# Optimization experiments

Measured on AMD Instinct MI355X. Metric: run time of the kernel, lower is better.

## Reference

```python
import jax, jax.numpy as jnp
import numpy as np

DEGREE = 12      # number of interior basis control dims
ORDER = 3        # cubic B-spline
V = 10           # number_variables
N = 65536        # batch
L = V * (V - 1) // 2          # 45 lambdas (strict lower triangle)
NCOEF = DEGREE + ORDER - 1    # 14 coefficients per lambda
LO, HI = -5.0, 5.0            # spline_range[:,0]


def make_knots():
    d = (HI - LO) / (DEGREE - 1)
    return jnp.linspace(LO - ORDER * d, HI + ORDER * d, DEGREE + 2 * ORDER, dtype=jnp.float32)


def bspline_basis(x, knots):
    # Cox-de Boor recursion, vectorized over all leading dims of x.
    # returns [..., NCOEF] basis values (len(knots) - ORDER - 1 functions).
    t = knots
    xe = x[..., None]
    B = ((xe >= t[:-1]) & (xe < t[1:])).astype(x.dtype)  # order-0 indicators
    for p in range(1, ORDER + 1):
        d1 = t[p:-1] - t[:-p - 1]
        d2 = t[p + 1:] - t[1:-p]
        a = jnp.where(d1 > 0, (xe - t[:-p - 1]) / jnp.where(d1 > 0, d1, 1.0), 0.0)
        b = jnp.where(d2 > 0, (t[p + 1:] - xe) / jnp.where(d2 > 0, d2, 1.0), 0.0)
        B = a * B[..., :-1] + b * B[..., 1:]
    return B


def setup_inputs() -> dict:
    key = jax.random.key(0)
    k1, k2 = jax.random.split(key)
    x = jax.random.normal(k1, (N, V), dtype=jnp.float32) * 2.0
    log_d = jnp.zeros((N, V), dtype=jnp.float32)
    params = 0.001 + 0.01 * jax.random.normal(k2, (NCOEF, L), dtype=jnp.float32)
    return {"x": x, "log_d": log_d, "params": params}


def reference(x, log_d, params):
    knots = make_knots()
    rows, cols = np.tril_indices(V, k=-1)  # var_num_list, covar_num_list
    # ReLULeR span restriction: clamp inputs into the spline range
    xc = jnp.clip(x[:, cols], LO, HI)              # [N, L]
    B = bspline_basis(xc, knots)                    # [N, L, NCOEF]
    lam = jnp.einsum('nlk,kl->nl', B, params)       # de Boor evaluation per pair
    # triangular lambda matrix: identity + scattered strict-lower entries
    eye = jnp.eye(V, dtype=x.dtype)
    M = jnp.broadcast_to(eye, (x.shape[0], V, V)).at[:, rows, cols].set(lam)
    out = jnp.einsum('nij,nj->ni', M, x)            # bmm(lambda_matrix, input)
    # ridge penalties on spline coefficients (penalize_towards=0)
    sec = jnp.sum(jnp.diff(params, n=2, axis=0) ** 2)
    fir = jnp.sum(jnp.diff(params, n=1, axis=0) ** 2)
    par = jnp.sum(params ** 2)
    return out, M, log_d, sec, fir, par
```

## Files before the change

### kernel.cpp

```cpp
#include <hip/hip_runtime.h>

#define V 10
#define L 45
#define NCOEF 14
#define NSAMP 65536
#define BS 32
#define LAMP 48

typedef float v4f __attribute__((ext_vector_type(4)));

__constant__ unsigned char c_col[L] = {
    0,
    0,1,
    0,1,2,
    0,1,2,3,
    0,1,2,3,4,
    0,1,2,3,4,5,
    0,1,2,3,4,5,6,
    0,1,2,3,4,5,6,7,
    0,1,2,3,4,5,6,7,8
};

__global__ __launch_bounds__(256) void decor_fused(
    const float* __restrict__ x, const float* __restrict__ log_d,
    const float* __restrict__ params,
    float* __restrict__ out, float* __restrict__ Mout, float* __restrict__ logd_out,
    float* __restrict__ scal)
{
    __shared__ float ps[NCOEF * L];
    __shared__ int   cols[L];
    __shared__ float xs[BS * V];
    __shared__ float lam[BS * LAMP];
    __shared__ float os[BS * V];

    const int tid = threadIdx.x;
    const int n0  = blockIdx.x * BS;

    for (int idx = tid; idx < NCOEF * L; idx += 256)
        ps[idx] = params[idx];
    if (tid < L) cols[tid] = c_col[tid];

    const v4f* x4 = (const v4f*)(x + (size_t)n0 * V);
    for (int idx = tid; idx < BS * V / 4; idx += 256)
        ((v4f*)xs)[idx] = __builtin_nontemporal_load(&x4[idx]);

    const v4f* ld4  = (const v4f*)(log_d + (size_t)n0 * V);
    v4f*       ldo4 = (v4f*)(logd_out + (size_t)n0 * V);
    for (int idx = tid; idx < BS * V / 4; idx += 256)
        __builtin_nontemporal_store(__builtin_nontemporal_load(&ld4[idx]), &ldo4[idx]);

    __syncthreads();

    const float inv_d = 1.1f;
    const float c16   = 1.0f / 6.0f;
    for (int idx = tid; idx < BS * L; idx += 256) {
        int nl = idx / L;
        int l  = idx - nl * L;
        float xv = xs[nl * V + cols[l]];
        xv = fminf(fmaxf(xv, -5.0f), 5.0f);
        float u  = (xv + 5.0f) * inv_d + 3.0f;
        int   ii = (int)floorf(u);
        ii = max(3, min(ii, 14));
        float f  = u - (float)ii;
        float omf = 1.0f - f;
        float f2 = f * f, f3 = f2 * f;
        float N0 = omf * omf * omf * c16;
        float N1 = (3.0f * f3 - 6.0f * f2 + 4.0f) * c16;
        float N2 = (-3.0f * f3 + 3.0f * f2 + 3.0f * f + 1.0f) * c16;
        float N3 = f3 * c16;
        int k0 = ii - 3;
        int k3 = min(k0 + 3, NCOEF - 1);
        lam[nl * LAMP + l] =
              N0 * ps[(k0    ) * L + l]
            + N1 * ps[(k0 + 1) * L + l]
            + N2 * ps[(k0 + 2) * L + l]
            + N3 * ps[(k3    ) * L + l];
    }
    __syncthreads();

    v4f* M4 = (v4f*)(Mout + (size_t)n0 * V * V);
    for (int idx = tid; idx < BS * 25; idx += 256) {
        int nl = idx / 25;
        int q  = idx - nl * 25;
        int e  = q * 4;
        const float* lr = &lam[nl * LAMP];
        v4f v;
        #pragma unroll
        for (int t = 0; t < 4; ++t) {
            int ee = e + t;
            int i  = (ee * 205) >> 11;
            int j  = ee - 10 * i;
            float val;
            if (j > i)       val = 0.0f;
            else if (j == i) val = 1.0f;
            else             val = lr[(i * (i - 1)) / 2 + j];
            v[t] = val;
        }
        __builtin_nontemporal_store(v, &M4[idx]);
    }

    for (int idx = tid; idx < BS * V; idx += 256) {
        int nl = idx / V;
        int i  = idx - nl * V;
        float acc = xs[idx];
        const float* lr = &lam[nl * LAMP + (i * (i - 1)) / 2];
        for (int j = 0; j < i; ++j)
            acc += lr[j] * xs[nl * V + j];
        os[idx] = acc;
    }
    __syncthreads();

    v4f* o4 = (v4f*)(out + (size_t)n0 * V);
    for (int idx = tid; idx < BS * V / 4; idx += 256)
        __builtin_nontemporal_store(((const v4f*)os)[idx], &o4[idx]);

    if (blockIdx.x == 0 && tid < 64) {
        float s_par = 0.f, s_fir = 0.f, s_sec = 0.f;
        for (int idx = tid; idx < NCOEF * L; idx += 64) {
            int k = idx / L;
            float p0 = ps[idx];
            s_par += p0 * p0;
            if (k + 1 < NCOEF) {
                float p1 = ps[idx + L];
                float d1 = p1 - p0;
                s_fir += d1 * d1;
                if (k + 2 < NCOEF) {
                    float p2 = ps[idx + 2 * L];
                    float d2 = p2 - 2.f * p1 + p0;
                    s_sec += d2 * d2;
                }
            }
        }
        for (int off = 32; off; off >>= 1) {
            s_sec += __shfl_down(s_sec, off);
            s_fir += __shfl_down(s_fir, off);
            s_par += __shfl_down(s_par, off);
        }
        if (tid == 0) { scal[0] = s_sec; scal[1] = s_fir; scal[2] = s_par; }
    }
}

extern "C" void kernel_launch(void* const* d_in, const int* in_sizes, int n_in,
                              void* d_out, int out_size, void* d_ws, size_t ws_size,
                              hipStream_t stream) {
    const float* x      = (const float*)d_in[0];
    const float* log_d  = (const float*)d_in[1];
    const float* params = (const float*)d_in[2];

    float* out      = (float*)d_out;
    float* M        = out + (size_t)NSAMP * V;
    float* logd_out = M + (size_t)NSAMP * V * V;
    float* scal     = logd_out + (size_t)NSAMP * V;

    decor_fused<<<NSAMP / BS, 256, 0, stream>>>(x, log_d, params, out, M, logd_out, scal);
}
```

Before: 17.75 us.

## Write M directly from lambda loop with scalar stores and halve block size

The vectorised M-matrix write pass is replaced by two kinds of scalar stores. The diagonal and upper-triangle constants are written up front, and each lambda is stored to M directly where it is computed. The output staging buffer and one barrier are removed, nontemporal loads and stores become plain accesses, and the block shrinks to 128 threads with an occupancy hint. This aims to cut a shared-memory pass and a sync. In exchange, the M stores become uncoalesced scalar writes instead of 16-byte vector stores, which may hurt write bandwidth on the dominant output.

```diff
diff --git a/kernel.cpp b/kernel.cpp
--- a/kernel.cpp
+++ b/kernel.cpp
@@ -5,58 +5,67 @@
 #define NCOEF 14
 #define NSAMP 65536
 #define BS 32
-#define LAMP 48
+#define NTHR 128
+#define LAMP 46
 
 typedef float v4f __attribute__((ext_vector_type(4)));
 
-__constant__ unsigned char c_col[L] = {
-    0,
-    0,1,
-    0,1,2,
-    0,1,2,3,
-    0,1,2,3,4,
-    0,1,2,3,4,5,
-    0,1,2,3,4,5,6,
-    0,1,2,3,4,5,6,7,
-    0,1,2,3,4,5,6,7,8
+__constant__ unsigned char c_ij[L] = {
+    0x10,
+    0x20,0x21,
+    0x30,0x31,0x32,
+    0x40,0x41,0x42,0x43,
+    0x50,0x51,0x52,0x53,0x54,
+    0x60,0x61,0x62,0x63,0x64,0x65,
+    0x70,0x71,0x72,0x73,0x74,0x75,0x76,
+    0x80,0x81,0x82,0x83,0x84,0x85,0x86,0x87,
+    0x90,0x91,0x92,0x93,0x94,0x95,0x96,0x97,0x98
 };
 
-__global__ __launch_bounds__(256) void decor_fused(
+__global__ __launch_bounds__(NTHR, 8) void decor_fused(
     const float* __restrict__ x, const float* __restrict__ log_d,
     const float* __restrict__ params,
     float* __restrict__ out, float* __restrict__ Mout, float* __restrict__ logd_out,
     float* __restrict__ scal)
 {
     __shared__ float ps[NCOEF * L];
-    __shared__ int   cols[L];
     __shared__ float xs[BS * V];
     __shared__ float lam[BS * LAMP];
-    __shared__ float os[BS * V];
+    __shared__ unsigned char ij[48];
 
     const int tid = threadIdx.x;
     const int n0  = blockIdx.x * BS;
+    float* __restrict__ Mb = Mout + (size_t)n0 * V * V;
 
-    for (int idx = tid; idx < NCOEF * L; idx += 256)
+    for (int idx = tid; idx < NCOEF * L; idx += NTHR)
         ps[idx] = params[idx];
-    if (tid < L) cols[tid] = c_col[tid];
+    const v4f* x4 = (const v4f*)(x + (size_t)n0 * V);
+    for (int idx = tid; idx < BS * V / 4; idx += NTHR)
+        ((v4f*)xs)[idx] = x4[idx];
+    if (tid < L) ij[tid] = c_ij[tid];
 
-    const v4f* x4 = (const v4f*)(x + (size_t)n0 * V);
-    for (int idx = tid; idx < BS * V / 4; idx += 256)
-        ((v4f*)xs)[idx] = __builtin_nontemporal_load(&x4[idx]);
+    for (int idx = tid; idx < BS * V * V; idx += NTHR) {
+        int e = idx % (V * V);
+        int i = (e * 205) >> 11;
+        int j = e - 10 * i;
+        if (j >= i) Mb[idx] = (j == i) ? 1.0f : 0.0f;
+    }
 
     const v4f* ld4  = (const v4f*)(log_d + (size_t)n0 * V);
     v4f*       ldo4 = (v4f*)(logd_out + (size_t)n0 * V);
-    for (int idx = tid; idx < BS * V / 4; idx += 256)
-        __builtin_nontemporal_store(__builtin_nontemporal_load(&ld4[idx]), &ldo4[idx]);
+    for (int idx = tid; idx < BS * V / 4; idx += NTHR)
+        ldo4[idx] = ld4[idx];
 
     __syncthreads();
 
     const float inv_d = 1.1f;
     const float c16   = 1.0f / 6.0f;
-    for (int idx = tid; idx < BS * L; idx += 256) {
+    for (int idx = tid; idx < BS * L; idx += NTHR) {
         int nl = idx / L;
         int l  = idx - nl * L;
-        float xv = xs[nl * V + cols[l]];
+        int pij = ij[l];
+        int i = pij >> 4, j = pij & 15;
+        float xv = xs[nl * V + j];
         xv = fminf(fmaxf(xv, -5.0f), 5.0f);
         float u  = (xv + 5.0f) * inv_d + 3.0f;
         int   ii = (int)floorf(u);
@@ -70,49 +79,26 @@
         float N3 = f3 * c16;
         int k0 = ii - 3;
         int k3 = min(k0 + 3, NCOEF - 1);
-        lam[nl * LAMP + l] =
+        float lv =
               N0 * ps[(k0    ) * L + l]
             + N1 * ps[(k0 + 1) * L + l]
             + N2 * ps[(k0 + 2) * L + l]
             + N3 * ps[(k3    ) * L + l];
+        lam[nl * LAMP + l] = lv;
+        Mb[nl * V * V + i * V + j] = lv;
     }
+
     __syncthreads();
 
-    v4f* M4 = (v4f*)(Mout + (size_t)n0 * V * V);
-    for (int idx = tid; idx < BS * 25; idx += 256) {
-        int nl = idx / 25;
-        int q  = idx - nl * 25;
-        int e  = q * 4;
-        const float* lr = &lam[nl * LAMP];
-        v4f v;
-        #pragma unroll
-        for (int t = 0; t < 4; ++t) {
-            int ee = e + t;
-            int i  = (ee * 205) >> 11;
-            int j  = ee - 10 * i;
-            float val;
-            if (j > i)       val = 0.0f;
-            else if (j == i) val = 1.0f;
-            else             val = lr[(i * (i - 1)) / 2 + j];
-            v[t] = val;
-        }
-        __builtin_nontemporal_store(v, &M4[idx]);
-    }
-
-    for (int idx = tid; idx < BS * V; idx += 256) {
+    for (int idx = tid; idx < BS * V; idx += NTHR) {
         int nl = idx / V;
         int i  = idx - nl * V;
         float acc = xs[idx];
         const float* lr = &lam[nl * LAMP + (i * (i - 1)) / 2];
         for (int j = 0; j < i; ++j)
             acc += lr[j] * xs[nl * V + j];
-        os[idx] = acc;
+        out[(size_t)n0 * V + idx] = acc;
     }
-    __syncthreads();
-
-    v4f* o4 = (v4f*)(out + (size_t)n0 * V);
-    for (int idx = tid; idx < BS * V / 4; idx += 256)
-        __builtin_nontemporal_store(((const v4f*)os)[idx], &o4[idx]);
 
     if (blockIdx.x == 0 && tid < 64) {
         float s_par = 0.f, s_fir = 0.f, s_sec = 0.f;
@@ -152,5 +138,5 @@
     float* logd_out = M + (size_t)NSAMP * V * V;
     float* scal     = logd_out + (size_t)NSAMP * V;
 
-    decor_fused<<<NSAMP / BS, 256, 0, stream>>>(x, log_d, params, out, M, logd_out, scal);
+    decor_fused<<<NSAMP / BS, NTHR, 0, stream>>>(x, log_d, params, out, M, logd_out, scal);
 }
```

New measurement: 20.12 us. +13.4%, slower.

## Fuse spline evaluation into M-matrix write and shrink blocks to 16 samples

Applied to the files above, without the earlier changes.

Computes each lambda inline while writing the M matrix and drops the separate lambda pass and one barrier. The output is now stored directly instead of being staged through shared memory. Block size drops from 32 to 16 samples with 128 threads, and launch bounds are set to allow more resident blocks. The aim is fewer barriers and lower shared-memory use per block, at the cost of twice as many blocks each reloading the params table and scalar, uncoalesced output stores.

```diff
diff --git a/kernel.cpp b/kernel.cpp
--- a/kernel.cpp
+++ b/kernel.cpp
@@ -4,86 +4,44 @@
 #define L 45
 #define NCOEF 14
 #define NSAMP 65536
-#define BS 32
-#define LAMP 48
+#define BS 16
+#define NTHR 128
+#define LAMP 46
 
 typedef float v4f __attribute__((ext_vector_type(4)));
 
-__constant__ unsigned char c_col[L] = {
-    0,
-    0,1,
-    0,1,2,
-    0,1,2,3,
-    0,1,2,3,4,
-    0,1,2,3,4,5,
-    0,1,2,3,4,5,6,
-    0,1,2,3,4,5,6,7,
-    0,1,2,3,4,5,6,7,8
-};
-
-__global__ __launch_bounds__(256) void decor_fused(
+__global__ __launch_bounds__(NTHR, 8) void decor_fused(
     const float* __restrict__ x, const float* __restrict__ log_d,
     const float* __restrict__ params,
     float* __restrict__ out, float* __restrict__ Mout, float* __restrict__ logd_out,
     float* __restrict__ scal)
 {
     __shared__ float ps[NCOEF * L];
-    __shared__ int   cols[L];
     __shared__ float xs[BS * V];
     __shared__ float lam[BS * LAMP];
-    __shared__ float os[BS * V];
 
     const int tid = threadIdx.x;
     const int n0  = blockIdx.x * BS;
 
-    for (int idx = tid; idx < NCOEF * L; idx += 256)
+    for (int idx = tid; idx < NCOEF * L; idx += NTHR)
         ps[idx] = params[idx];
-    if (tid < L) cols[tid] = c_col[tid];
-
     const v4f* x4 = (const v4f*)(x + (size_t)n0 * V);
-    for (int idx = tid; idx < BS * V / 4; idx += 256)
+    for (int idx = tid; idx < BS * V / 4; idx += NTHR)
         ((v4f*)xs)[idx] = __builtin_nontemporal_load(&x4[idx]);
-
     const v4f* ld4  = (const v4f*)(log_d + (size_t)n0 * V);
     v4f*       ldo4 = (v4f*)(logd_out + (size_t)n0 * V);
-    for (int idx = tid; idx < BS * V / 4; idx += 256)
+    for (int idx = tid; idx < BS * V / 4; idx += NTHR)
         __builtin_nontemporal_store(__builtin_nontemporal_load(&ld4[idx]), &ldo4[idx]);
 
     __syncthreads();
 
     const float inv_d = 1.1f;
     const float c16   = 1.0f / 6.0f;
-    for (int idx = tid; idx < BS * L; idx += 256) {
-        int nl = idx / L;
-        int l  = idx - nl * L;
-        float xv = xs[nl * V + cols[l]];
-        xv = fminf(fmaxf(xv, -5.0f), 5.0f);
-        float u  = (xv + 5.0f) * inv_d + 3.0f;
-        int   ii = (int)floorf(u);
-        ii = max(3, min(ii, 14));
-        float f  = u - (float)ii;
-        float omf = 1.0f - f;
-        float f2 = f * f, f3 = f2 * f;
-        float N0 = omf * omf * omf * c16;
-        float N1 = (3.0f * f3 - 6.0f * f2 + 4.0f) * c16;
-        float N2 = (-3.0f * f3 + 3.0f * f2 + 3.0f * f + 1.0f) * c16;
-        float N3 = f3 * c16;
-        int k0 = ii - 3;
-        int k3 = min(k0 + 3, NCOEF - 1);
-        lam[nl * LAMP + l] =
-              N0 * ps[(k0    ) * L + l]
-            + N1 * ps[(k0 + 1) * L + l]
-            + N2 * ps[(k0 + 2) * L + l]
-            + N3 * ps[(k3    ) * L + l];
-    }
-    __syncthreads();
-
     v4f* M4 = (v4f*)(Mout + (size_t)n0 * V * V);
-    for (int idx = tid; idx < BS * 25; idx += 256) {
+    for (int idx = tid; idx < BS * 25; idx += NTHR) {
         int nl = idx / 25;
         int q  = idx - nl * 25;
         int e  = q * 4;
-        const float* lr = &lam[nl * LAMP];
         v4f v;
         #pragma unroll
         for (int t = 0; t < 4; ++t) {
@@ -93,26 +51,43 @@
             float val;
             if (j > i)       val = 0.0f;
             else if (j == i) val = 1.0f;
-            else             val = lr[(i * (i - 1)) / 2 + j];
+            else {
+                float xv = xs[nl * V + j];
+                xv = fminf(fmaxf(xv, -5.0f), 5.0f);
+                float u  = (xv + 5.0f) * inv_d + 3.0f;
+                int   ii = (int)floorf(u);
+                ii = max(3, min(ii, 14));
+                float f  = u - (float)ii;
+                float omf = 1.0f - f;
+                float f2 = f * f, f3 = f2 * f;
+                float N0 = omf * omf * omf * c16;
+                float N1 = (3.0f * f3 - 6.0f * f2 + 4.0f) * c16;
+                float N2 = (-3.0f * f3 + 3.0f * f2 + 3.0f * f + 1.0f) * c16;
+                float N3 = f3 * c16;
+                int l  = (i * (i - 1)) / 2 + j;
+                int k0 = ii - 3;
+                int k3 = min(k0 + 3, NCOEF - 1);
+                val = N0 * ps[(k0    ) * L + l]
+                    + N1 * ps[(k0 + 1) * L + l]
+                    + N2 * ps[(k0 + 2) * L + l]
+                    + N3 * ps[(k3    ) * L + l];
+                lam[nl * LAMP + l] = val;
+            }
             v[t] = val;
         }
         __builtin_nontemporal_store(v, &M4[idx]);
     }
+    __syncthreads();
 
-    for (int idx = tid; idx < BS * V; idx += 256) {
+    for (int idx = tid; idx < BS * V; idx += NTHR) {
         int nl = idx / V;
         int i  = idx - nl * V;
         float acc = xs[idx];
         const float* lr = &lam[nl * LAMP + (i * (i - 1)) / 2];
         for (int j = 0; j < i; ++j)
             acc += lr[j] * xs[nl * V + j];
-        os[idx] = acc;
+        __builtin_nontemporal_store(acc, &out[(size_t)n0 * V + idx]);
     }
-    __syncthreads();
-
-    v4f* o4 = (v4f*)(out + (size_t)n0 * V);
-    for (int idx = tid; idx < BS * V / 4; idx += 256)
-        __builtin_nontemporal_store(((const v4f*)os)[idx], &o4[idx]);
 
     if (blockIdx.x == 0 && tid < 64) {
         float s_par = 0.f, s_fir = 0.f, s_sec = 0.f;
@@ -152,5 +127,5 @@
     float* logd_out = M + (size_t)NSAMP * V * V;
     float* scal     = logd_out + (size_t)NSAMP * V;
 
-    decor_fused<<<NSAMP / BS, 256, 0, stream>>>(x, log_d, params, out, M, logd_out, scal);
+    decor_fused<<<NSAMP / BS, NTHR, 0, stream>>>(x, log_d, params, out, M, logd_out, scal);
 }
```

After: 21.26 us. 19.8% more time.

## Give each wavefront its own sample slice to drop block-wide barriers

Applied to the files above, without the earlier changes.

Block size rises to 64 samples, split into four 16-sample slices, one per wavefront. Each wave loads its own x slice and writes its own lambda buffer in shared memory, so only one block barrier remains (the one after the params and x load). The output staging buffer is removed and out is written directly with scalar nontemporal stores, which gives up the vectorized v4f output stores. The lambda row pitch shrinks to 46, the grid is halved, and block 0's fourth wave now computes the penalty sums.

```diff
diff --git a/kernel.cpp b/kernel.cpp
--- a/kernel.cpp
+++ b/kernel.cpp
@@ -4,8 +4,10 @@
 #define L 45
 #define NCOEF 14
 #define NSAMP 65536
-#define BS 32
-#define LAMP 48
+#define BS 64
+#define SPW 16
+#define NTHR 256
+#define LAMP 46
 
 typedef float v4f __attribute__((ext_vector_type(4)));
 
@@ -21,42 +23,44 @@
     0,1,2,3,4,5,6,7,8
 };
 
-__global__ __launch_bounds__(256) void decor_fused(
+__global__ __launch_bounds__(NTHR) void decor_fused(
     const float* __restrict__ x, const float* __restrict__ log_d,
     const float* __restrict__ params,
     float* __restrict__ out, float* __restrict__ Mout, float* __restrict__ logd_out,
     float* __restrict__ scal)
 {
     __shared__ float ps[NCOEF * L];
-    __shared__ int   cols[L];
-    __shared__ float xs[BS * V];
-    __shared__ float lam[BS * LAMP];
-    __shared__ float os[BS * V];
+    __shared__ unsigned char cols[64];
+    __shared__ float xs[4][SPW * V];
+    __shared__ float lam[4][SPW * LAMP];
 
-    const int tid = threadIdx.x;
-    const int n0  = blockIdx.x * BS;
+    const int tid  = threadIdx.x;
+    const int w    = tid >> 6;
+    const int lane = tid & 63;
+    const size_t nw = (size_t)blockIdx.x * BS + w * SPW;
 
-    for (int idx = tid; idx < NCOEF * L; idx += 256)
+    for (int idx = tid; idx < NCOEF * L; idx += NTHR)
         ps[idx] = params[idx];
     if (tid < L) cols[tid] = c_col[tid];
 
-    const v4f* x4 = (const v4f*)(x + (size_t)n0 * V);
-    for (int idx = tid; idx < BS * V / 4; idx += 256)
-        ((v4f*)xs)[idx] = __builtin_nontemporal_load(&x4[idx]);
-
-    const v4f* ld4  = (const v4f*)(log_d + (size_t)n0 * V);
-    v4f*       ldo4 = (v4f*)(logd_out + (size_t)n0 * V);
-    for (int idx = tid; idx < BS * V / 4; idx += 256)
-        __builtin_nontemporal_store(__builtin_nontemporal_load(&ld4[idx]), &ldo4[idx]);
+    const v4f* x4w = (const v4f*)(x + nw * V);
+    if (lane < SPW * V / 4)
+        ((v4f*)xs[w])[lane] = __builtin_nontemporal_load(&x4w[lane]);
+    const v4f* ld4w  = (const v4f*)(log_d + nw * V);
+    v4f*       ldo4w = (v4f*)(logd_out + nw * V);
+    if (lane < SPW * V / 4)
+        __builtin_nontemporal_store(__builtin_nontemporal_load(&ld4w[lane]), &ldo4w[lane]);
 
     __syncthreads();
 
     const float inv_d = 1.1f;
     const float c16   = 1.0f / 6.0f;
-    for (int idx = tid; idx < BS * L; idx += 256) {
-        int nl = idx / L;
-        int l  = idx - nl * L;
-        float xv = xs[nl * V + cols[l]];
+    float* lamw = lam[w];
+    const float* xw = xs[w];
+    for (int e = lane; e < SPW * L; e += 64) {
+        int nl = e / L;
+        int l  = e - nl * L;
+        float xv = xw[nl * V + cols[l]];
         xv = fminf(fmaxf(xv, -5.0f), 5.0f);
         float u  = (xv + 5.0f) * inv_d + 3.0f;
         int   ii = (int)floorf(u);
@@ -70,24 +74,23 @@
         float N3 = f3 * c16;
         int k0 = ii - 3;
         int k3 = min(k0 + 3, NCOEF - 1);
-        lam[nl * LAMP + l] =
+        lamw[nl * LAMP + l] =
               N0 * ps[(k0    ) * L + l]
             + N1 * ps[(k0 + 1) * L + l]
             + N2 * ps[(k0 + 2) * L + l]
             + N3 * ps[(k3    ) * L + l];
     }
-    __syncthreads();
 
-    v4f* M4 = (v4f*)(Mout + (size_t)n0 * V * V);
-    for (int idx = tid; idx < BS * 25; idx += 256) {
-        int nl = idx / 25;
-        int q  = idx - nl * 25;
-        int e  = q * 4;
-        const float* lr = &lam[nl * LAMP];
+    v4f* M4w = (v4f*)(Mout + nw * V * V);
+    for (int q = lane; q < SPW * 25; q += 64) {
+        int nl = q / 25;
+        int qq = q - nl * 25;
+        int e0 = qq * 4;
+        const float* lr = &lamw[nl * LAMP];
         v4f v;
         #pragma unroll
         for (int t = 0; t < 4; ++t) {
-            int ee = e + t;
+            int ee = e0 + t;
             int i  = (ee * 205) >> 11;
             int j  = ee - 10 * i;
             float val;
@@ -96,27 +99,22 @@
             else             val = lr[(i * (i - 1)) / 2 + j];
             v[t] = val;
         }
-        __builtin_nontemporal_store(v, &M4[idx]);
+        __builtin_nontemporal_store(v, &M4w[q]);
     }
 
-    for (int idx = tid; idx < BS * V; idx += 256) {
-        int nl = idx / V;
-        int i  = idx - nl * V;
-        float acc = xs[idx];
-        const float* lr = &lam[nl * LAMP + (i * (i - 1)) / 2];
+    for (int o = lane; o < SPW * V; o += 64) {
+        int nl = o / V;
+        int i  = o - nl * V;
+        float acc = xw[o];
+        const float* lr = &lamw[nl * LAMP + (i * (i - 1)) / 2];
         for (int j = 0; j < i; ++j)
-            acc += lr[j] * xs[nl * V + j];
-        os[idx] = acc;
+            acc += lr[j] * xw[nl * V + j];
+        __builtin_nontemporal_store(acc, &out[nw * V + o]);
     }
-    __syncthreads();
 
-    v4f* o4 = (v4f*)(out + (size_t)n0 * V);
-    for (int idx = tid; idx < BS * V / 4; idx += 256)
-        __builtin_nontemporal_store(((const v4f*)os)[idx], &o4[idx]);
-
-    if (blockIdx.x == 0 && tid < 64) {
+    if (blockIdx.x == 0 && w == 3) {
         float s_par = 0.f, s_fir = 0.f, s_sec = 0.f;
-        for (int idx = tid; idx < NCOEF * L; idx += 64) {
+        for (int idx = lane; idx < NCOEF * L; idx += 64) {
             int k = idx / L;
             float p0 = ps[idx];
             s_par += p0 * p0;
@@ -136,7 +134,7 @@
             s_fir += __shfl_down(s_fir, off);
             s_par += __shfl_down(s_par, off);
         }
-        if (tid == 0) { scal[0] = s_sec; scal[1] = s_fir; scal[2] = s_par; }
+        if (lane == 0) { scal[0] = s_sec; scal[1] = s_fir; scal[2] = s_par; }
     }
 }
 
@@ -152,5 +150,5 @@
     float* logd_out = M + (size_t)NSAMP * V * V;
     float* scal     = logd_out + (size_t)NSAMP * V;
 
-    decor_fused<<<NSAMP / BS, 256, 0, stream>>>(x, log_d, params, out, M, logd_out, scal);
+    decor_fused<<<NSAMP / BS, NTHR, 0, stream>>>(x, log_d, params, out, M, logd_out, scal);
 }
```

Result: slower. 19.71 us (+11.1%).
